# Performance work log

Measured on AMD Instinct MI355X. Metric: run time of the kernel, lower is better.

Reference implementation:

```python
import jax, jax.numpy as jnp
import numpy as np

N_HEADS = 16
LEVELS = 3
DS = 2          # downsampling_factor
WINDOW = 128    # sliding window size
B, L, E = 32, 512, 1024


def _mha(q, k, v, Wq, bq, Wk, bk, Wv, bv, Wo, bo):
    """batch_first nn.MultiheadAttention equivalent (no mask)."""
    b, lq, e = q.shape
    lk = k.shape[1]
    d = e // N_HEADS
    scale = 1.0 / np.sqrt(d)
    qh = (q @ Wq + bq).reshape(b, lq, N_HEADS, d)
    kh = (k @ Wk + bk).reshape(b, lk, N_HEADS, d)
    vh = (v @ Wv + bv).reshape(b, lk, N_HEADS, d)
    att = jax.nn.softmax(jnp.einsum('bqhd,bkhd->bhqk', qh, kh) * scale, axis=-1)
    out = jnp.einsum('bhqk,bkhd->bqhd', att, vh).reshape(b, lq, e)
    return out @ Wo + bo


def _downsample(x):
    b, l, e = x.shape
    ln = l // DS
    return x[:, :ln * DS].reshape(b, ln, DS, e).mean(axis=2)


def setup_inputs() -> dict:
    key = jax.random.key(0)
    ks = jax.random.split(key, 8)
    s = E ** -0.5
    return {
        'query': jax.random.normal(ks[0], (B, L, E), jnp.float32),
        'key': jax.random.normal(ks[1], (B, L, E), jnp.float32),
        'value': jax.random.normal(ks[2], (B, L, E), jnp.float32),
        'Wq': jax.random.normal(ks[3], (E, E), jnp.float32) * s,
        'bq': jnp.zeros((E,), jnp.float32),
        'Wk': jax.random.normal(ks[4], (E, E), jnp.float32) * s,
        'bk': jnp.zeros((E,), jnp.float32),
        'Wv': jax.random.normal(ks[5], (E, E), jnp.float32) * s,
        'bv': jnp.zeros((E,), jnp.float32),
        'Wo': jax.random.normal(ks[6], (E, E), jnp.float32) * s,
        'bo': jnp.zeros((E,), jnp.float32),
        'soft_mask': jnp.ones((L,), jnp.float32),
    }


def reference(query, key, value, Wq, bq, Wk, bk, Wv, bv, Wo, bo, soft_mask):
    params = (Wq, bq, Wk, bk, Wv, bv, Wo, bo)
    # hierarchical multi-scale attention: full KV + (levels-1) downsampled KVs
    k, v = key, value
    acc = _mha(query, k, v, *params)
    for _ in range(LEVELS - 1):
        k = _downsample(k)
        v = _downsample(v)
        acc = acc + _mha(query, k, v, *params)
    hier = acc / LEVELS
    # sliding-window local attention (L divisible by WINDOW)
    b, l, e = query.shape
    nw = l // WINDOW
    qw = query.reshape(b * nw, WINDOW, e)
    kw = key.reshape(b * nw, WINDOW, e)
    vw = value.reshape(b * nw, WINDOW, e)
    sw = _mha(qw, kw, vw, *params).reshape(b, l, e)
    # soft mask gating
    sm = jax.nn.sigmoid(soft_mask[:l])
    return (hier + sw) * sm[None, :, None]
```

## Files before the change

kernel.cpp:

```cpp
#include <hip/hip_runtime.h>

#define EDIM 1024
#define MROWS 16384
#define DHEAD 64
#define LSEQ 512

typedef unsigned short u16;
typedef unsigned int u32;
typedef __bf16 bf16x8 __attribute__((ext_vector_type(8)));
typedef unsigned short u16x8 __attribute__((ext_vector_type(8)));
typedef float f32x4 __attribute__((ext_vector_type(4)));

__device__ __forceinline__ u16 f2bf(float x) {
    return __builtin_bit_cast(u16, (__bf16)x);
}
__device__ __forceinline__ float bf2f(u16 h) {
    return __builtin_bit_cast(float, (u32)h << 16);
}
__device__ __forceinline__ bf16x8 ld8(const u16* p) {
    return __builtin_bit_cast(bf16x8, *(const u16x8*)p);
}
__device__ __forceinline__ bf16x8 ld8s(const u16* base, int row, int koff) {
    return ld8((const u16*)((const char*)base + row * 128 + ((koff * 2) ^ ((row & 7) << 4))));
}
__device__ __forceinline__ bf16x8 ld8v(const u16* base, int c, int koff) {
    return ld8((const u16*)((const char*)base + c * 128 + ((koff * 2) ^ (((c >> 2) & 7) << 4))));
}
__device__ __forceinline__ void glds16(const u16* g, u16* l) {
    __builtin_amdgcn_global_load_lds(
        (const __attribute__((address_space(1))) u32*)g,
        (__attribute__((address_space(3))) u32*)l, 16, 0, 0);
}
#define MFMA(a, b, c) __builtin_amdgcn_mfma_f32_16x16x32_bf16((a), (b), (c), 0, 0, 0)
#define U4C(v, i) ((i) == 0 ? (v).x : (i) == 1 ? (v).y : (i) == 2 ? (v).z : (v).w)

__global__ __launch_bounds__(256) void prep_wt_kernel(
    const float* __restrict__ Wq, const float* __restrict__ Wk,
    const float* __restrict__ Wv, const float* __restrict__ Wo,
    u16* __restrict__ WTh)
{
    const int z = blockIdx.z;
    const float* W = (z == 0) ? Wq : (z == 1) ? Wk : (z == 2) ? Wv : Wo;
    u16* th = WTh + (size_t)z * EDIM * EDIM;
    const int k0 = blockIdx.x * 64, n0 = blockIdx.y * 64;
    __shared__ float tile[64][65];
    for (int i = threadIdx.x; i < 4096; i += 256) {
        int r = i >> 6, c = i & 63;
        tile[r][c] = W[(size_t)(k0 + r) * EDIM + n0 + c];
    }
    __syncthreads();
    for (int i = threadIdx.x; i < 4096; i += 256) {
        int r = i >> 6, c = i & 63;
        th[(size_t)(n0 + r) * EDIM + k0 + c] = f2bf(tile[c][r]);
    }
}

__global__ __launch_bounds__(256, 3) void gemm_proj(
    const float* __restrict__ Aq, const float* __restrict__ Ak, const float* __restrict__ Av,
    const u16* __restrict__ WT,
    const float* __restrict__ bq, const float* __restrict__ bk, const float* __restrict__ bv,
    u16* __restrict__ Cq, u16* __restrict__ Ck, u16* __restrict__ Cv)
{
    const int z = blockIdx.z;
    const float* A = (z == 0) ? Aq : (z == 1) ? Ak : Av;
    const u16* BT = WT + (size_t)z * EDIM * EDIM;
    const float* bias = (z == 0) ? bq : (z == 1) ? bk : bv;
    u16* C = (z == 0) ? Cq : (z == 1) ? Ck : Cv;

    const int tid = threadIdx.x;
    const int lane = tid & 63, w = tid >> 6;
    const int wm = w >> 1, wn = w & 1;
    const int lr = lane & 15, lg = lane >> 4;
    int D = blockIdx.y * gridDim.x + blockIdx.x;
    int T = (D & 7) * 128 + (D >> 3);
    const int m0 = (T >> 3) * 128, n0 = (T & 7) * 128;

    __shared__ u16 As[128 * 64];
    __shared__ u16 Bs[128 * 64];

    f32x4 acc[4][4] = {};
    float4 ar[8];
    #pragma unroll
    for (int j = 0; j < 8; ++j) {
        int i4 = tid + j * 256;
        int r = i4 >> 4, c4 = (i4 & 15) << 2;
        ar[j] = *(const float4*)&A[(size_t)(m0 + r) * EDIM + c4];
    }

    for (int k0 = 0; k0 < EDIM; k0 += 64) {
        #pragma unroll
        for (int c = 0; c < 4; ++c) {
            int idx = tid + c * 256;
            int row = idx >> 3, ch = idx & 7;
            int sch = ch ^ (row & 7);
            glds16(&BT[(size_t)(n0 + row) * EDIM + k0 + sch * 8],
                   &Bs[(w * 64 + c * 256) * 8]);
        }
        #pragma unroll
        for (int j = 0; j < 8; ++j) {
            int i4 = tid + j * 256;
            int r = i4 >> 4, c4 = (i4 & 15) << 2;
            float4 v = ar[j];
            ushort4 hv;
            hv.x = f2bf(v.x); hv.y = f2bf(v.y); hv.z = f2bf(v.z); hv.w = f2bf(v.w);
            *(ushort4*)((char*)As + r * 128 + ((c4 * 2) ^ ((r & 7) << 4))) = hv;
        }
        if (k0 + 64 < EDIM) {
            #pragma unroll
            for (int j = 0; j < 8; ++j) {
                int i4 = tid + j * 256;
                int r = i4 >> 4, c4 = (i4 & 15) << 2;
                ar[j] = *(const float4*)&A[(size_t)(m0 + r) * EDIM + k0 + 64 + c4];
            }
        }
        __syncthreads();
        #pragma unroll
        for (int ks = 0; ks < 2; ++ks) {
            const int koff = ks * 32 + lg * 8;
            bf16x8 ah[4];
            #pragma unroll
            for (int m = 0; m < 4; ++m)
                ah[m] = ld8s(As, wm * 64 + m * 16 + lr, koff);
            #pragma unroll
            for (int n = 0; n < 4; ++n) {
                bf16x8 bh = ld8s(Bs, wn * 64 + n * 16 + lr, koff);
                #pragma unroll
                for (int m = 0; m < 4; ++m)
                    acc[m][n] = MFMA(ah[m], bh, acc[m][n]);
            }
        }
        __syncthreads();
    }
    #pragma unroll
    for (int m = 0; m < 4; ++m)
        #pragma unroll
        for (int n = 0; n < 4; ++n) {
            int col = n0 + wn * 64 + n * 16 + lr;
            float bc = bias[col];
            #pragma unroll
            for (int r = 0; r < 4; ++r) {
                int row = m0 + wm * 64 + m * 16 + lg * 4 + r;
                C[(size_t)row * EDIM + col] = f2bf(acc[m][n][r] + bc);
            }
        }
}

__global__ __launch_bounds__(256, 3) void gemm_out(
    const u16* __restrict__ Actx, const u16* __restrict__ BT,
    const float* __restrict__ bias,
    float* __restrict__ Cf, const float* __restrict__ smask)
{
    const int tid = threadIdx.x;
    const int lane = tid & 63, w = tid >> 6;
    const int wm = w >> 1, wn = w & 1;
    const int lr = lane & 15, lg = lane >> 4;
    int D = blockIdx.y * gridDim.x + blockIdx.x;
    int T = (D & 7) * 128 + (D >> 3);
    const int m0 = (T >> 3) * 128, n0 = (T & 7) * 128;

    __shared__ u16 As[128 * 64];
    __shared__ u16 Bs[128 * 64];

    f32x4 acc[4][4] = {};
    for (int k0 = 0; k0 < EDIM; k0 += 64) {
        #pragma unroll
        for (int c = 0; c < 4; ++c) {
            int idx = tid + c * 256;
            int row = idx >> 3, ch = idx & 7;
            int sch = ch ^ (row & 7);
            glds16(&Actx[(size_t)(m0 + row) * EDIM + k0 + sch * 8],
                   &As[(w * 64 + c * 256) * 8]);
            glds16(&BT[(size_t)(n0 + row) * EDIM + k0 + sch * 8],
                   &Bs[(w * 64 + c * 256) * 8]);
        }
        __syncthreads();
        #pragma unroll
        for (int ks = 0; ks < 2; ++ks) {
            const int koff = ks * 32 + lg * 8;
            bf16x8 ah[4];
            #pragma unroll
            for (int m = 0; m < 4; ++m)
                ah[m] = ld8s(As, wm * 64 + m * 16 + lr, koff);
            #pragma unroll
            for (int n = 0; n < 4; ++n) {
                bf16x8 bh = ld8s(Bs, wn * 64 + n * 16 + lr, koff);
                #pragma unroll
                for (int m = 0; m < 4; ++m)
                    acc[m][n] = MFMA(ah[m], bh, acc[m][n]);
            }
        }
        __syncthreads();
    }
    #pragma unroll
    for (int m = 0; m < 4; ++m)
        #pragma unroll
        for (int n = 0; n < 4; ++n) {
            int col = n0 + wn * 64 + n * 16 + lr;
            float bc = bias[col];
            #pragma unroll
            for (int r = 0; r < 4; ++r) {
                int row = m0 + wm * 64 + m * 16 + lg * 4 + r;
                float g = 1.0f / (1.0f + __expf(-smask[row & (LSEQ - 1)]));
                Cf[(size_t)row * EDIM + col] = (acc[m][n][r] + 2.0f * bc) * g;
            }
        }
}

__global__ __launch_bounds__(256, 2) void attn_kernel(
    const u16* __restrict__ Q, const u16* __restrict__ K,
    const u16* __restrict__ V, u16* __restrict__ ctx)
{
    const int tid = threadIdx.x, lane = tid & 63, w = tid >> 6;
    const int lr = lane & 15, lg = lane >> 4;
    int D = (blockIdx.z * gridDim.y + blockIdx.y) * gridDim.x + blockIdx.x;
    int T = (D & 7) * 512 + (D >> 3);
    const int qq = T & 7, hd = (T >> 3) & 15, b = T >> 7;
    const int wrow = b * LSEQ + qq * 64 + w * 16;
    const int ecol = hd * DHEAD;
    const int kvbase = b * LSEQ;
    const int wt0 = qq & ~1;

    __shared__ u16 Ks[2][64 * 64];
    __shared__ u16 Vt[64 * 64];
    __shared__ u16 Ps[4][3 * 16 * 72];

    u16* psw = &Ps[w][0];

    bf16x8 qf0 = ld8(&Q[(size_t)(wrow + lr) * EDIM + ecol + lg * 8]);
    bf16x8 qf1 = ld8(&Q[(size_t)(wrow + lr) * EDIM + ecol + 32 + lg * 8]);

    f32x4 o0[4] = {}, o1[4] = {}, o2[4] = {}, ow[4] = {};
    float l0 = 0, l1 = 0, l2 = 0, lw = 0;
    ushort4 vr[2][2];

    auto issueK = [&](int t, int bf) {
        #pragma unroll
        for (int c = 0; c < 2; ++c) {
            int idx = tid + c * 256;
            int row = idx >> 3, ch = idx & 7;
            int sch = ch ^ (row & 7);
            glds16(&K[(size_t)(kvbase + t * 64 + row) * EDIM + ecol + sch * 8],
                   &Ks[bf][(w * 64 + c * 256) * 8]);
        }
    };
    auto loadV = [&](int t) {
        #pragma unroll
        for (int j = 0; j < 2; ++j) {
            int i4 = tid + j * 256;
            int pr = i4 >> 4, c4 = (i4 & 15) << 2;
            vr[j][0] = *(const ushort4*)&V[(size_t)(kvbase + t * 64 + 2 * pr) * EDIM + ecol + c4];
            vr[j][1] = *(const ushort4*)&V[(size_t)(kvbase + t * 64 + 2 * pr + 1) * EDIM + ecol + c4];
        }
    };
    auto writeV = [&]() {
        #pragma unroll
        for (int j = 0; j < 2; ++j) {
            int i4 = tid + j * 256;
            int pr = i4 >> 4, c4 = (i4 & 15) << 2;
            #pragma unroll
            for (int i = 0; i < 4; ++i) {
                int c = c4 + i;
                int byo = c * 128 + ((4 * pr) ^ (((c >> 2) & 7) << 4));
                *(u32*)((char*)Vt + byo) =
                    (u32)U4C(vr[j][0], i) | ((u32)U4C(vr[j][1], i) << 16);
            }
        }
    };

    int buf = 0;
    issueK(0, 0);
    loadV(0);
    for (int t = 0; t < 8; ++t) {
        __syncthreads();
        writeV();
        __syncthreads();
        if (t < 7) { issueK(t + 1, buf ^ 1); loadV(t + 1); }
        const bool win = (t == wt0) | (t == wt0 + 1);

        float l0t = 0;
        #pragma unroll
        for (int nb = 0; nb < 4; ++nb) {
            bf16x8 kf0 = ld8s(&Ks[buf][0], nb * 16 + lr, lg * 8);
            bf16x8 kf1 = ld8s(&Ks[buf][0], nb * 16 + lr, 32 + lg * 8);
            f32x4 s = {};
            s = MFMA(kf0, qf0, s);
            s = MFMA(kf1, qf1, s);
            s *= 0.125f;
            float p00 = __expf(s[0]), p01 = __expf(s[1]);
            float p02 = __expf(s[2]), p03 = __expf(s[3]);
            float s1a = 0.5f * (s[0] + s[1]), s1b = 0.5f * (s[2] + s[3]);
            float p1a = 0.5f * __expf(s1a), p1b = 0.5f * __expf(s1b);
            float p2v = 0.25f * __expf(0.5f * (s1a + s1b));
            l0t += (p00 + p01) + (p02 + p03);
            l1 += 2.0f * (p1a + p1b);
            l2 += 4.0f * p2v;
            int rb = lr * 144 + nb * 32 + lg * 8;
            *(u32*)((char*)psw + rb)     = (u32)f2bf(p00) | ((u32)f2bf(p01) << 16);
            *(u32*)((char*)psw + rb + 4) = (u32)f2bf(p02) | ((u32)f2bf(p03) << 16);
            u32 w1a = (u32)f2bf(p1a); w1a |= w1a << 16;
            u32 w1b = (u32)f2bf(p1b); w1b |= w1b << 16;
            *(u32*)((char*)psw + 2304 + rb)     = w1a;
            *(u32*)((char*)psw + 2304 + rb + 4) = w1b;
            u32 w2 = (u32)f2bf(p2v); w2 |= w2 << 16;
            *(u32*)((char*)psw + 4608 + rb)     = w2;
            *(u32*)((char*)psw + 4608 + rb + 4) = w2;
        }
        l0 += l0t;
        if (win) lw += l0t;

        bf16x8 pa00 = ld8((const u16*)((char*)psw + lr * 144 + lg * 16));
        bf16x8 pa01 = ld8((const u16*)((char*)psw + lr * 144 + 64 + lg * 16));
        bf16x8 pa10 = ld8((const u16*)((char*)psw + 2304 + lr * 144 + lg * 16));
        bf16x8 pa11 = ld8((const u16*)((char*)psw + 2304 + lr * 144 + 64 + lg * 16));
        bf16x8 pa20 = ld8((const u16*)((char*)psw + 4608 + lr * 144 + lg * 16));
        bf16x8 pa21 = ld8((const u16*)((char*)psw + 4608 + lr * 144 + 64 + lg * 16));
        #pragma unroll
        for (int nd = 0; nd < 4; ++nd) {
            bf16x8 vb0 = ld8v(Vt, nd * 16 + lr, lg * 8);
            bf16x8 vb1 = ld8v(Vt, nd * 16 + lr, 32 + lg * 8);
            o0[nd] = MFMA(pa00, vb0, o0[nd]); o0[nd] = MFMA(pa01, vb1, o0[nd]);
            o1[nd] = MFMA(pa10, vb0, o1[nd]); o1[nd] = MFMA(pa11, vb1, o1[nd]);
            o2[nd] = MFMA(pa20, vb0, o2[nd]); o2[nd] = MFMA(pa21, vb1, o2[nd]);
            if (win) {
                ow[nd] = MFMA(pa00, vb0, ow[nd]);
                ow[nd] = MFMA(pa01, vb1, ow[nd]);
            }
        }
        buf ^= 1;
    }
    l0 += __shfl_xor(l0, 16, 64); l0 += __shfl_xor(l0, 32, 64);
    l1 += __shfl_xor(l1, 16, 64); l1 += __shfl_xor(l1, 32, 64);
    l2 += __shfl_xor(l2, 16, 64); l2 += __shfl_xor(l2, 32, 64);
    lw += __shfl_xor(lw, 16, 64); lw += __shfl_xor(lw, 32, 64);
    float c0 = (1.0f / 3.0f) / l0, c1 = (1.0f / 3.0f) / l1;
    float c2 = (1.0f / 3.0f) / l2, cw = 1.0f / lw;
    #pragma unroll
    for (int r = 0; r < 4; ++r) {
        int src = lg * 4 + r;
        float d0 = __shfl(c0, src, 64);
        float d1 = __shfl(c1, src, 64);
        float d2 = __shfl(c2, src, 64);
        float dw = __shfl(cw, src, 64);
        #pragma unroll
        for (int nd = 0; nd < 4; ++nd) {
            float v = o0[nd][r] * d0 + o1[nd][r] * d1 + o2[nd][r] * d2 + ow[nd][r] * dw;
            ctx[(size_t)(wrow + lg * 4 + r) * EDIM + ecol + nd * 16 + lr] = f2bf(v);
        }
    }
}

extern "C" void kernel_launch(void* const* d_in, const int* in_sizes, int n_in,
                              void* d_out, int out_size, void* d_ws, size_t ws_size,
                              hipStream_t stream)
{
    const float* query = (const float*)d_in[0];
    const float* key   = (const float*)d_in[1];
    const float* value = (const float*)d_in[2];
    const float* Wq = (const float*)d_in[3];
    const float* bq = (const float*)d_in[4];
    const float* Wk = (const float*)d_in[5];
    const float* bk = (const float*)d_in[6];
    const float* Wv = (const float*)d_in[7];
    const float* bv = (const float*)d_in[8];
    const float* Wo = (const float*)d_in[9];
    const float* bo = (const float*)d_in[10];
    const float* smask = (const float*)d_in[11];

    const size_t szWT = (size_t)4 * EDIM * EDIM * 2;
    const size_t szP  = (size_t)MROWS * EDIM * 2;
    const size_t need = szWT + 4 * szP;
    if (ws_size < need) {
        hipMemsetAsync(d_out, 0x7F, (size_t)out_size * 4, stream);
        return;
    }
    size_t off = 0;
    auto take = [&](size_t n) -> void* {
        void* p = (char*)d_ws + off;
        off += (n + 255) & ~(size_t)255;
        return p;
    };
    u16* WTh = (u16*)take(szWT);
    u16* Qh  = (u16*)take(szP);
    u16* Kh  = (u16*)take(szP);
    u16* Vh  = (u16*)take(szP);
    u16* ctx = (u16*)take(szP);

    prep_wt_kernel<<<dim3(16, 16, 4), 256, 0, stream>>>(Wq, Wk, Wv, Wo, WTh);

    gemm_proj<<<dim3(8, 128, 3), 256, 0, stream>>>(
        query, key, value, WTh, bq, bk, bv, Qh, Kh, Vh);

    attn_kernel<<<dim3(8, 16, 32), 256, 0, stream>>>(Qh, Kh, Vh, ctx);

    gemm_out<<<dim3(8, 128), 256, 0, stream>>>(
        ctx, WTh + 3 * (size_t)EDIM * EDIM, bo, (float*)d_out, smask);
}
```

Before: 341.6 us.

## Replace projection GEMMs with double-buffered 256x256 tile GEMM and separate fp32->bf16 conversion

Converts query/key/value from fp32 to bf16 in a standalone pass, then runs all four projections through a new 512-thread 256x256-tile GEMM. The new GEMM double-buffers A and B in 128KB of LDS, loads both via global_load_lds, and interleaves MFMA bursts with LDS fragment loads under explicit barriers, vmcnt waits and setprio. The aim is better data reuse per tile and overlap of global loads with MFMA. In exchange it adds an extra HBM round trip for the bf16 copies, uses three more workspace buffers, and runs only 256 blocks at one block per CU.

```diff
diff --git a/kernel.cpp b/kernel.cpp
--- a/kernel.cpp
+++ b/kernel.cpp
@@ -4,6 +4,7 @@
 #define MROWS 16384
 #define DHEAD 64
 #define LSEQ 512
+#define NT 16
 
 typedef unsigned short u16;
 typedef unsigned int u32;
@@ -33,6 +34,8 @@
 }
 #define MFMA(a, b, c) __builtin_amdgcn_mfma_f32_16x16x32_bf16((a), (b), (c), 0, 0, 0)
 #define U4C(v, i) ((i) == 0 ? (v).x : (i) == 1 ? (v).y : (i) == 2 ? (v).z : (v).w)
+#define VMCNT(n) asm volatile("s_waitcnt vmcnt(" #n ")" ::: "memory")
+#define SBAR()   __builtin_amdgcn_s_barrier()
 
 __global__ __launch_bounds__(256) void prep_wt_kernel(
     const float* __restrict__ Wq, const float* __restrict__ Wk,
@@ -55,153 +58,160 @@
     }
 }
 
-__global__ __launch_bounds__(256, 3) void gemm_proj(
+__global__ __launch_bounds__(256) void convert_kernel(
     const float* __restrict__ Aq, const float* __restrict__ Ak, const float* __restrict__ Av,
-    const u16* __restrict__ WT,
-    const float* __restrict__ bq, const float* __restrict__ bk, const float* __restrict__ bv,
-    u16* __restrict__ Cq, u16* __restrict__ Ck, u16* __restrict__ Cv)
+    u16* __restrict__ Dq, u16* __restrict__ Dk, u16* __restrict__ Dv)
 {
     const int z = blockIdx.z;
-    const float* A = (z == 0) ? Aq : (z == 1) ? Ak : Av;
-    const u16* BT = WT + (size_t)z * EDIM * EDIM;
-    const float* bias = (z == 0) ? bq : (z == 1) ? bk : bv;
-    u16* C = (z == 0) ? Cq : (z == 1) ? Ck : Cv;
-
+    const float* src = (z == 0) ? Aq : (z == 1) ? Ak : Av;
+    u16* dst = (z == 0) ? Dq : (z == 1) ? Dk : Dv;
+    const size_t total8 = (size_t)MROWS * EDIM / 8;
+    for (size_t i = (size_t)blockIdx.x * 256 + threadIdx.x; i < total8;
+         i += (size_t)gridDim.x * 256) {
+        const float4 a = *(const float4*)&src[i * 8];
+        const float4 b = *(const float4*)&src[i * 8 + 4];
+        ushort4 h0, h1;
+        h0.x = f2bf(a.x); h0.y = f2bf(a.y); h0.z = f2bf(a.z); h0.w = f2bf(a.w);
+        h1.x = f2bf(b.x); h1.y = f2bf(b.y); h1.z = f2bf(b.z); h1.w = f2bf(b.w);
+        *(ushort4*)&dst[i * 8]     = h0;
+        *(ushort4*)&dst[i * 8 + 4] = h1;
+    }
+}
+
+template<int EPI>
+__global__ __launch_bounds__(512, 1) void gemm256(
+    const u16* __restrict__ A, const u16* __restrict__ BT,
+    const float* __restrict__ bias,
+    u16* __restrict__ Ch, float* __restrict__ Cf, const float* __restrict__ smask)
+{
+    extern __shared__ u16 lds[];
     const int tid = threadIdx.x;
     const int lane = tid & 63, w = tid >> 6;
-    const int wm = w >> 1, wn = w & 1;
+    const int wm = w >> 2, wn = w & 3;
     const int lr = lane & 15, lg = lane >> 4;
-    int D = blockIdx.y * gridDim.x + blockIdx.x;
-    int T = (D & 7) * 128 + (D >> 3);
-    const int m0 = (T >> 3) * 128, n0 = (T & 7) * 128;
-
-    __shared__ u16 As[128 * 64];
-    __shared__ u16 Bs[128 * 64];
-
-    f32x4 acc[4][4] = {};
-    float4 ar[8];
+    int D = blockIdx.x;
+    int T = (D & 7) * 32 + (D >> 3);
+    const int m0 = (T >> 2) * 256, n0 = (T & 3) * 256;
+
+    u16* As0 = lds;
+    u16* As1 = lds + 16384;
+    u16* Bs0 = lds + 32768;
+    u16* Bs1 = lds + 49152;
+
+    auto stageB = [&](int bf, int t) {
+        u16* dst = bf ? Bs1 : Bs0;
+        #pragma unroll
+        for (int c = 0; c < 4; ++c) {
+            int idx = tid + c * 512;
+            int row = idx >> 3, ch = idx & 7, sch = ch ^ (row & 7);
+            glds16(&BT[(size_t)(n0 + row) * EDIM + t * 64 + sch * 8], dst + idx * 8);
+        }
+    };
+    auto stageA = [&](int bf, int t) {
+        u16* dst = bf ? As1 : As0;
+        #pragma unroll
+        for (int c = 0; c < 4; ++c) {
+            int idx = tid + c * 512;
+            int row = idx >> 3, ch = idx & 7, sch = ch ^ (row & 7);
+            glds16(&A[(size_t)(m0 + row) * EDIM + t * 64 + sch * 8], dst + idx * 8);
+        }
+    };
+
+    f32x4 acc[8][4] = {};
+    bf16x8 bf0[4], bf1[4];
+
+    stageB(0, 0);
+    stageA(0, 0);
+    VMCNT(0);
+    SBAR();
     #pragma unroll
-    for (int j = 0; j < 8; ++j) {
-        int i4 = tid + j * 256;
-        int r = i4 >> 4, c4 = (i4 & 15) << 2;
-        ar[j] = *(const float4*)&A[(size_t)(m0 + r) * EDIM + c4];
-    }
-
-    for (int k0 = 0; k0 < EDIM; k0 += 64) {
-        #pragma unroll
-        for (int c = 0; c < 4; ++c) {
-            int idx = tid + c * 256;
-            int row = idx >> 3, ch = idx & 7;
-            int sch = ch ^ (row & 7);
-            glds16(&BT[(size_t)(n0 + row) * EDIM + k0 + sch * 8],
-                   &Bs[(w * 64 + c * 256) * 8]);
-        }
-        #pragma unroll
-        for (int j = 0; j < 8; ++j) {
-            int i4 = tid + j * 256;
-            int r = i4 >> 4, c4 = (i4 & 15) << 2;
-            float4 v = ar[j];
-            ushort4 hv;
-            hv.x = f2bf(v.x); hv.y = f2bf(v.y); hv.z = f2bf(v.z); hv.w = f2bf(v.w);
-            *(ushort4*)((char*)As + r * 128 + ((c4 * 2) ^ ((r & 7) << 4))) = hv;
-        }
-        if (k0 + 64 < EDIM) {
-            #pragma unroll
-            for (int j = 0; j < 8; ++j) {
-                int i4 = tid + j * 256;
-                int r = i4 >> 4, c4 = (i4 & 15) << 2;
-                ar[j] = *(const float4*)&A[(size_t)(m0 + r) * EDIM + k0 + 64 + c4];
-            }
-        }
-        __syncthreads();
-        #pragma unroll
-        for (int ks = 0; ks < 2; ++ks) {
-            const int koff = ks * 32 + lg * 8;
-            bf16x8 ah[4];
-            #pragma unroll
-            for (int m = 0; m < 4; ++m)
-                ah[m] = ld8s(As, wm * 64 + m * 16 + lr, koff);
-            #pragma unroll
-            for (int n = 0; n < 4; ++n) {
-                bf16x8 bh = ld8s(Bs, wn * 64 + n * 16 + lr, koff);
-                #pragma unroll
-                for (int m = 0; m < 4; ++m)
-                    acc[m][n] = MFMA(ah[m], bh, acc[m][n]);
-            }
-        }
-        __syncthreads();
+    for (int n = 0; n < 4; ++n)
+        bf0[n] = ld8s(Bs0, wn * 64 + n * 16 + lr, lg * 8);
+
+    for (int t = 0; t < NT; ++t) {
+        const int cur = t & 1;
+        u16* Asc = cur ? As1 : As0;
+        u16* Bsc = cur ? Bs1 : Bs0;
+        u16* Bsn = cur ? Bs0 : Bs1;
+        const bool more = (t + 1 < NT);
+        bf16x8 af[4];
+        #pragma unroll
+        for (int mm = 0; mm < 4; ++mm)
+            af[mm] = ld8s(Asc, wm * 128 + mm * 16 + lr, lg * 8);
+        if (more) { stageB(cur ^ 1, t + 1); stageA(cur ^ 1, t + 1); }
+        SBAR();
+        __builtin_amdgcn_s_setprio(1);
+        #pragma unroll
+        for (int n = 0; n < 4; ++n)
+            #pragma unroll
+            for (int mm = 0; mm < 4; ++mm)
+                acc[mm][n] = MFMA(af[mm], bf0[n], acc[mm][n]);
+        __builtin_amdgcn_s_setprio(0);
+        SBAR();
+        bf16x8 ag[4];
+        #pragma unroll
+        for (int mm = 0; mm < 4; ++mm)
+            ag[mm] = ld8s(Asc, wm * 128 + 64 + mm * 16 + lr, lg * 8);
+        SBAR();
+        __builtin_amdgcn_s_setprio(1);
+        #pragma unroll
+        for (int n = 0; n < 4; ++n)
+            #pragma unroll
+            for (int mm = 0; mm < 4; ++mm)
+                acc[4 + mm][n] = MFMA(ag[mm], bf0[n], acc[4 + mm][n]);
+        __builtin_amdgcn_s_setprio(0);
+        SBAR();
+        #pragma unroll
+        for (int mm = 0; mm < 4; ++mm)
+            af[mm] = ld8s(Asc, wm * 128 + mm * 16 + lr, 32 + lg * 8);
+        #pragma unroll
+        for (int n = 0; n < 4; ++n)
+            bf1[n] = ld8s(Bsc, wn * 64 + n * 16 + lr, 32 + lg * 8);
+        SBAR();
+        __builtin_amdgcn_s_setprio(1);
+        #pragma unroll
+        for (int n = 0; n < 4; ++n)
+            #pragma unroll
+            for (int mm = 0; mm < 4; ++mm)
+                acc[mm][n] = MFMA(af[mm], bf1[n], acc[mm][n]);
+        __builtin_amdgcn_s_setprio(0);
+        VMCNT(4);
+        SBAR();
+        #pragma unroll
+        for (int mm = 0; mm < 4; ++mm)
+            ag[mm] = ld8s(Asc, wm * 128 + 64 + mm * 16 + lr, 32 + lg * 8);
+        if (more) {
+            #pragma unroll
+            for (int n = 0; n < 4; ++n)
+                bf0[n] = ld8s(Bsn, wn * 64 + n * 16 + lr, lg * 8);
+        }
+        SBAR();
+        __builtin_amdgcn_s_setprio(1);
+        #pragma unroll
+        for (int n = 0; n < 4; ++n)
+            #pragma unroll
+            for (int mm = 0; mm < 4; ++mm)
+                acc[4 + mm][n] = MFMA(ag[mm], bf1[n], acc[4 + mm][n]);
+        __builtin_amdgcn_s_setprio(0);
+        VMCNT(0);
+        SBAR();
     }
     #pragma unroll
-    for (int m = 0; m < 4; ++m)
+    for (int m = 0; m < 8; ++m)
         #pragma unroll
         for (int n = 0; n < 4; ++n) {
             int col = n0 + wn * 64 + n * 16 + lr;
             float bc = bias[col];
             #pragma unroll
             for (int r = 0; r < 4; ++r) {
-                int row = m0 + wm * 64 + m * 16 + lg * 4 + r;
-                C[(size_t)row * EDIM + col] = f2bf(acc[m][n][r] + bc);
-            }
-        }
-}
-
-__global__ __launch_bounds__(256, 3) void gemm_out(
-    const u16* __restrict__ Actx, const u16* __restrict__ BT,
-    const float* __restrict__ bias,
-    float* __restrict__ Cf, const float* __restrict__ smask)
-{
-    const int tid = threadIdx.x;
-    const int lane = tid & 63, w = tid >> 6;
-    const int wm = w >> 1, wn = w & 1;
-    const int lr = lane & 15, lg = lane >> 4;
-    int D = blockIdx.y * gridDim.x + blockIdx.x;
-    int T = (D & 7) * 128 + (D >> 3);
-    const int m0 = (T >> 3) * 128, n0 = (T & 7) * 128;
-
-    __shared__ u16 As[128 * 64];
-    __shared__ u16 Bs[128 * 64];
-
-    f32x4 acc[4][4] = {};
-    for (int k0 = 0; k0 < EDIM; k0 += 64) {
-        #pragma unroll
-        for (int c = 0; c < 4; ++c) {
-            int idx = tid + c * 256;
-            int row = idx >> 3, ch = idx & 7;
-            int sch = ch ^ (row & 7);
-            glds16(&Actx[(size_t)(m0 + row) * EDIM + k0 + sch * 8],
-                   &As[(w * 64 + c * 256) * 8]);
-            glds16(&BT[(size_t)(n0 + row) * EDIM + k0 + sch * 8],
-                   &Bs[(w * 64 + c * 256) * 8]);
-        }
-        __syncthreads();
-        #pragma unroll
-        for (int ks = 0; ks < 2; ++ks) {
-            const int koff = ks * 32 + lg * 8;
-            bf16x8 ah[4];
-            #pragma unroll
-            for (int m = 0; m < 4; ++m)
-                ah[m] = ld8s(As, wm * 64 + m * 16 + lr, koff);
-            #pragma unroll
-            for (int n = 0; n < 4; ++n) {
-                bf16x8 bh = ld8s(Bs, wn * 64 + n * 16 + lr, koff);
-                #pragma unroll
-                for (int m = 0; m < 4; ++m)
-                    acc[m][n] = MFMA(ah[m], bh, acc[m][n]);
-            }
-        }
-        __syncthreads();
-    }
-    #pragma unroll
-    for (int m = 0; m < 4; ++m)
-        #pragma unroll
-        for (int n = 0; n < 4; ++n) {
-            int col = n0 + wn * 64 + n * 16 + lr;
-            float bc = bias[col];
-            #pragma unroll
-            for (int r = 0; r < 4; ++r) {
-                int row = m0 + wm * 64 + m * 16 + lg * 4 + r;
-                float g = 1.0f / (1.0f + __expf(-smask[row & (LSEQ - 1)]));
-                Cf[(size_t)row * EDIM + col] = (acc[m][n][r] + 2.0f * bc) * g;
+                int row = m0 + wm * 128 + m * 16 + lg * 4 + r;
+                float x = acc[m][n][r];
+                if (EPI == 1) {
+                    float g = 1.0f / (1.0f + __expf(-smask[row & (LSEQ - 1)]));
+                    Cf[(size_t)row * EDIM + col] = (x + 2.0f * bc) * g;
+                } else {
+                    Ch[(size_t)row * EDIM + col] = f2bf(x + bc);
+                }
             }
         }
 }
@@ -368,7 +378,7 @@
 
     const size_t szWT = (size_t)4 * EDIM * EDIM * 2;
     const size_t szP  = (size_t)MROWS * EDIM * 2;
-    const size_t need = szWT + 4 * szP;
+    const size_t need = szWT + 7 * szP;
     if (ws_size < need) {
         hipMemsetAsync(d_out, 0x7F, (size_t)out_size * 4, stream);
         return;
@@ -380,18 +390,31 @@
         return p;
     };
     u16* WTh = (u16*)take(szWT);
+    u16* Aq  = (u16*)take(szP);
+    u16* Ak  = (u16*)take(szP);
+    u16* Av  = (u16*)take(szP);
     u16* Qh  = (u16*)take(szP);
     u16* Kh  = (u16*)take(szP);
     u16* Vh  = (u16*)take(szP);
     u16* ctx = (u16*)take(szP);
 
+    hipFuncSetAttribute(reinterpret_cast<const void*>(gemm256<0>),
+                        hipFuncAttributeMaxDynamicSharedMemorySize, 131072);
+    hipFuncSetAttribute(reinterpret_cast<const void*>(gemm256<1>),
+                        hipFuncAttributeMaxDynamicSharedMemorySize, 131072);
+
     prep_wt_kernel<<<dim3(16, 16, 4), 256, 0, stream>>>(Wq, Wk, Wv, Wo, WTh);
-
-    gemm_proj<<<dim3(8, 128, 3), 256, 0, stream>>>(
-        query, key, value, WTh, bq, bk, bv, Qh, Kh, Vh);
+    convert_kernel<<<dim3(4096, 1, 3), 256, 0, stream>>>(query, key, value, Aq, Ak, Av);
+
+    gemm256<0><<<256, 512, 131072, stream>>>(
+        Aq, WTh + 0 * (size_t)EDIM * EDIM, bq, Qh, nullptr, nullptr);
+    gemm256<0><<<256, 512, 131072, stream>>>(
+        Ak, WTh + 1 * (size_t)EDIM * EDIM, bk, Kh, nullptr, nullptr);
+    gemm256<0><<<256, 512, 131072, stream>>>(
+        Av, WTh + 2 * (size_t)EDIM * EDIM, bv, Vh, nullptr, nullptr);
 
     attn_kernel<<<dim3(8, 16, 32), 256, 0, stream>>>(Qh, Kh, Vh, ctx);
 
-    gemm_out<<<dim3(8, 128), 256, 0, stream>>>(
-        ctx, WTh + 3 * (size_t)EDIM * EDIM, bo, (float*)d_out, smask);
-}
+    gemm256<1><<<256, 512, 131072, stream>>>(
+        ctx, WTh + 3 * (size_t)EDIM * EDIM, bo, nullptr, (float*)d_out, smask);
+}
```

Result: slower. 377.7 us (+10.6%).
